# Kernel optimization log

Hardware: AMD Instinct MI355X
Metric: run time of the kernel (lower is better)

Reference implementation:

```python
import jax, jax.numpy as jnp
import numpy as np
import math

HQ, HKV, DH, WIN = 16, 4, 128, 512
RMS_EPS = 1.1920929e-07  # torch F.rms_norm default eps = fp32 machine eps


def _apply_rope(x, cos, sin):
    # x: [B,H,T,Dh]; interleaved-pair rotation as in the torch code
    x_even = x[..., ::2]
    x_odd = x[..., 1::2]
    x_rot = jnp.stack((-x_odd, x_even), axis=-1).reshape(x.shape)
    return x * cos + x_rot * sin


def _rms_norm(x):
    return x * jax.lax.rsqrt(jnp.mean(x * x, axis=-1, keepdims=True) + RMS_EPS)


def setup_inputs() -> dict:
    key = jax.random.key(0)
    k1, k2, k3 = jax.random.split(key, 3)
    B, T, C = 2, 2048, 2048
    x = jax.random.normal(k1, (B, T, C), dtype=jnp.float32)
    w_qkv = jax.random.normal(k2, ((HQ + 2 * HKV) * DH, C), dtype=jnp.float32) * 0.02
    w_proj = jax.random.normal(k3, (C, C), dtype=jnp.float32) * 0.02
    return {"x": x, "w_qkv": w_qkv, "w_proj": w_proj}


def reference(x, w_qkv, w_proj):
    B, T, C = x.shape
    rep = HQ // HKV
    qkv = x @ w_qkv.T  # [B,T,(Hq+2Hkv)*Dh]
    q, k, v = jnp.split(qkv, [HQ * DH, (HQ + HKV) * DH], axis=-1)
    Q = q.reshape(B, T, HQ, DH).transpose(0, 2, 1, 3)   # [B,Hq,T,Dh]
    K = k.reshape(B, T, HKV, DH).transpose(0, 2, 1, 3)  # [B,Hkv,T,Dh]
    V = v.reshape(B, T, HKV, DH).transpose(0, 2, 1, 3)
    # GQA expansion (repeat_interleave on head dim)
    K = jnp.repeat(K, rep, axis=1)
    V = jnp.repeat(V, rep, axis=1)
    # RoPE tables: freqs [T, Dh/2] -> cos/sin [1,1,T,Dh] via repeat_interleave(2)
    inv_freq = 1.0 / (10000.0 ** (jnp.arange(0, DH, 2, dtype=jnp.float32) / DH))
    freqs = jnp.arange(T, dtype=jnp.float32)[:, None] * inv_freq[None, :]
    cos = jnp.repeat(jnp.cos(freqs), 2, axis=-1)[None, None]
    sin = jnp.repeat(jnp.sin(freqs), 2, axis=-1)[None, None]
    Q = _rms_norm(_apply_rope(Q, cos, sin))
    K = _rms_norm(_apply_rope(K, cos, sin))
    scores = jnp.einsum('bhqd,bhkd->bhqk', Q, K) / math.sqrt(DH)
    i = jnp.arange(T)[:, None]
    j = jnp.arange(T)[None, :]
    mask = (i >= j) & ((i - j) < WIN)  # causal sliding window
    scores = jnp.where(mask[None, None], scores, -jnp.inf)
    attn = jax.nn.softmax(scores, axis=-1)
    y = jnp.einsum('bhqk,bhkd->bhqd', attn, V)
    y = y.transpose(0, 2, 1, 3).reshape(B, T, C)
    return y @ w_proj.T
```

## Files before the change

### kernel.cpp

```cpp
#include <hip/hip_runtime.h>
#include <stdint.h>

#define T_SEQ 2048
#define NB    2
#define DHD   128
#define NHQ   16
#define NHKV  4
#define SWIN  512
#define CDIM  2048
#define QKVN  3072
#define GBK   32

typedef __attribute__((ext_vector_type(8))) short short8;
typedef __attribute__((ext_vector_type(4))) float f32x4;
typedef __attribute__((ext_vector_type(16))) float f32x16;
typedef __attribute__((ext_vector_type(4))) unsigned int u32x4;
typedef __attribute__((address_space(3))) unsigned int lds_u32;
typedef __attribute__((address_space(1))) const unsigned int gbl_u32;

__device__ __forceinline__ unsigned short f2bf(float f) {
  unsigned int u = __float_as_uint(f);
  u += 0x7fffu + ((u >> 16) & 1u);
  return (unsigned short)(u >> 16);
}
__device__ __forceinline__ float bf2f(unsigned int h) {
  return __uint_as_float(h << 16);
}
__device__ __forceinline__ float exp2_fast(float x) {
  float r;
  asm("v_exp_f32 %0, %1" : "=v"(r) : "v"(x));
  return r;
}

__global__ __launch_bounds__(256) void k_f2bf3(const float* __restrict__ a, unsigned short* __restrict__ oa, int na4,
                                               const float* __restrict__ b, unsigned short* __restrict__ ob, int nb4,
                                               const float* __restrict__ c, unsigned short* __restrict__ oc, int nc4) {
  const int n = na4 + nb4 + nc4;
  for (int i = blockIdx.x * 256 + threadIdx.x; i < n; i += gridDim.x * 256) {
    const float* src; unsigned short* dst; int j = i;
    if (j < na4) { src = a; dst = oa; }
    else if (j < na4 + nb4) { j -= na4; src = b; dst = ob; }
    else { j -= na4 + nb4; src = c; dst = oc; }
    float4 v = reinterpret_cast<const float4*>(src)[j];
    uint2 o;
    o.x = ((unsigned int)f2bf(v.y) << 16) | f2bf(v.x);
    o.y = ((unsigned int)f2bf(v.w) << 16) | f2bf(v.z);
    reinterpret_cast<uint2*>(dst)[j] = o;
  }
}

__global__ __launch_bounds__(256) void k_trig(float* __restrict__ tbl) {
  int i = blockIdx.x * 256 + threadIdx.x;
  if (i >= T_SEQ * 64) return;
  int t = i >> 6, f = i & 63;
  float invf = powf(10000.f, -(float)f * (1.f / 64.f));
  float ang = (float)t * invf;
  tbl[i] = cosf(ang);
  tbl[T_SEQ * 64 + i] = sinf(ang);
}

template<int OUT_BF16>
__global__ __launch_bounds__(512, 2) void k_gemm192(const unsigned short* __restrict__ A,
                                                    const unsigned short* __restrict__ B,
                                                    void* __restrict__ Cout,
                                                    int M, int N, int K, int nbx) {
  extern __shared__ __align__(16) char lds[];
  const int tid = threadIdx.x, lane = tid & 63, wid = tid >> 6;
  const int lr = lane & 15, lg = lane >> 4;
  const int wr = wid >> 2, wcn = wid & 3;

  const int nwg = gridDim.x, cpx = nwg >> 3;
  const int id = (int)blockIdx.x;
  const int sid = (id & 7) * cpx + (id >> 3);
  const int by = sid / nbx, bx = sid - by * nbx;

  const unsigned short* Ab = A + (size_t)by * 256 * K;
  const unsigned short* Bb = B + (size_t)bx * 192 * K;

  const int row0 = tid >> 2;
  const int blk  = tid & 3;
  const int col0 = ((blk * 16) ^ (((row0 >> 1) & 3) << 4)) >> 1;
  const unsigned short* pA0 = Ab + (size_t)row0 * K + col0;
  const unsigned short* pA1 = pA0 + (size_t)128 * K;
  const unsigned short* pB0 = Bb + (size_t)row0 * K + col0;
  const unsigned short* pB2 = pB0 + (size_t)128 * K;

  const int sw  = ((lg ^ ((lr >> 1) & 3)) << 4);
  const int arb = (wr * 128 + lr) * 64 + sw;
  const int brb = 16384 + (wcn * 48 + lr) * 64 + sw;

  f32x4 acc[8][3];
#pragma unroll
  for (int mi = 0; mi < 8; ++mi)
#pragma unroll
    for (int ni = 0; ni < 3; ++ni)
#pragma unroll
      for (int r = 0; r < 4; ++r) acc[mi][ni][r] = 0.f;

#define STAGE(t) do {                                                                  \
    const int sl_ = (t) & 3; const int ko_ = (t) * GBK;                                \
    char* sb_ = lds + sl_ * 28672;                                                     \
    __builtin_amdgcn_global_load_lds((gbl_u32*)(pA0 + ko_),                            \
        (lds_u32*)(sb_ + wid * 1024), 16, 0, 0);                                       \
    __builtin_amdgcn_global_load_lds((gbl_u32*)(pA1 + ko_),                            \
        (lds_u32*)(sb_ + 8192 + wid * 1024), 16, 0, 0);                                \
    __builtin_amdgcn_global_load_lds((gbl_u32*)(pB0 + ko_),                            \
        (lds_u32*)(sb_ + 16384 + wid * 1024), 16, 0, 0);                               \
    if (wid < 4)                                                                       \
      __builtin_amdgcn_global_load_lds((gbl_u32*)(pB2 + ko_),                          \
          (lds_u32*)(sb_ + 24576 + wid * 1024), 16, 0, 0);                             \
  } while (0)

#define COMPUTE(t) do {                                                                \
    const int sl_ = (t) & 3;                                                           \
    const char* sb_ = lds + sl_ * 28672;                                               \
    short8 afr[8], bfr[3];                                                             \
    _Pragma("unroll") for (int mi = 0; mi < 8; ++mi)                                   \
      afr[mi] = *reinterpret_cast<const short8*>(sb_ + arb + mi * 1024);               \
    _Pragma("unroll") for (int ni = 0; ni < 3; ++ni)                                   \
      bfr[ni] = *reinterpret_cast<const short8*>(sb_ + brb + ni * 1024);               \
    __builtin_amdgcn_s_setprio(1);                                                     \
    _Pragma("unroll") for (int mi = 0; mi < 8; ++mi)                                   \
      _Pragma("unroll") for (int ni = 0; ni < 3; ++ni)                                 \
        acc[mi][ni] = __builtin_amdgcn_mfma_f32_16x16x32_bf16(afr[mi], bfr[ni],        \
                                                              acc[mi][ni], 0, 0, 0);   \
    __builtin_amdgcn_s_setprio(0);                                                     \
  } while (0)

#define WAITBAR2(nlo, nhi) do {                                                        \
    if (wid < 4) asm volatile("s_waitcnt vmcnt(" #nlo ")" ::: "memory");               \
    else         asm volatile("s_waitcnt vmcnt(" #nhi ")" ::: "memory");               \
    __builtin_amdgcn_s_barrier();                                                      \
    asm volatile("" ::: "memory");                                                     \
  } while (0)

  const int nt = K / GBK;
  STAGE(0); STAGE(1); STAGE(2);
  for (int t = 0; t < nt - 3; ++t) {
    WAITBAR2(10, 8);
    STAGE(t + 3);
    COMPUTE(t);
  }
  WAITBAR2(10, 8); COMPUTE(nt - 3);
  WAITBAR2(5, 4);  COMPUTE(nt - 2);
  WAITBAR2(0, 0);  COMPUTE(nt - 1);

#undef STAGE
#undef COMPUTE
#undef WAITBAR2

#pragma unroll
  for (int mi = 0; mi < 8; ++mi) {
    const int row0c = by * 256 + wr * 128 + mi * 16 + lg * 4;
#pragma unroll
    for (int ni = 0; ni < 3; ++ni) {
      const int col = bx * 192 + wcn * 48 + ni * 16 + lr;
#pragma unroll
      for (int r = 0; r < 4; ++r) {
        size_t idx = (size_t)(row0c + r) * N + col;
        if (OUT_BF16) ((unsigned short*)Cout)[idx] = f2bf(acc[mi][ni][r]);
        else          ((float*)Cout)[idx] = acc[mi][ni][r];
      }
    }
  }
}

template<int OUT_BF16>
__global__ __launch_bounds__(512) void k_gemm128(const unsigned short* __restrict__ A,
                                                 const unsigned short* __restrict__ B,
                                                 void* __restrict__ Cout,
                                                 int M, int N, int K, int nbx) {
  extern __shared__ __align__(16) char lds[];
  const int tid = threadIdx.x, lane = tid & 63, wid = tid >> 6;
  const int lr = lane & 15, lg = lane >> 4;
  const int wr = wid >> 2, wcn = wid & 3;

  const int nwg = gridDim.x, cpx = nwg >> 3;
  const int id = (int)blockIdx.x;
  const int sid = (id & 7) * cpx + (id >> 3);
  const int by = sid / nbx, bx = sid - by * nbx;

  const unsigned short* Ab = A + (size_t)by * 128 * K;
  const unsigned short* Bb = B + (size_t)bx * 256 * K;

  const int row0 = tid >> 2;
  const int blk  = tid & 3;
  const int col0 = ((blk * 16) ^ (((row0 >> 1) & 3) << 4)) >> 1;
  const unsigned short* pA0 = Ab + (size_t)row0 * K + col0;
  const unsigned short* pB0 = Bb + (size_t)row0 * K + col0;
  const unsigned short* pB1 = pB0 + (size_t)128 * K;

  const int sw  = ((lg ^ ((lr >> 1) & 3)) << 4);
  const int arb = (wr * 64 + lr) * 64 + sw;
  const int brb = (wcn * 64 + lr) * 64 + sw;

  f32x4 acc[4][4];
#pragma unroll
  for (int mi = 0; mi < 4; ++mi)
#pragma unroll
    for (int ni = 0; ni < 4; ++ni)
#pragma unroll
      for (int r = 0; r < 4; ++r) acc[mi][ni][r] = 0.f;

#define STAGE(t, sl_) do {                                                             \
    const int ko_ = (t) * GBK;                                                         \
    __builtin_amdgcn_global_load_lds((gbl_u32*)(pA0 + ko_),                            \
        (lds_u32*)(lds + (sl_) * 24576 + wid * 1024), 16, 0, 0);                       \
    __builtin_amdgcn_global_load_lds((gbl_u32*)(pB0 + ko_),                            \
        (lds_u32*)(lds + (sl_) * 24576 + 8192 + wid * 1024), 16, 0, 0);                \
    __builtin_amdgcn_global_load_lds((gbl_u32*)(pB1 + ko_),                            \
        (lds_u32*)(lds + (sl_) * 24576 + 16384 + wid * 1024), 16, 0, 0);               \
  } while (0)

#define COMPUTE(sl_) do {                                                              \
    const char* As_ = lds + (sl_) * 24576;                                             \
    const char* Bs_ = As_ + 8192;                                                      \
    short8 afr[4], bfr[4];                                                             \
    _Pragma("unroll") for (int mi = 0; mi < 4; ++mi)                                   \
      afr[mi] = *reinterpret_cast<const short8*>(As_ + arb + mi * 1024);               \
    _Pragma("unroll") for (int ni = 0; ni < 4; ++ni)                                   \
      bfr[ni] = *reinterpret_cast<const short8*>(Bs_ + brb + ni * 1024);               \
    __builtin_amdgcn_s_setprio(1);                                                     \
    _Pragma("unroll") for (int mi = 0; mi < 4; ++mi)                                   \
      _Pragma("unroll") for (int ni = 0; ni < 4; ++ni)                                 \
        acc[mi][ni] = __builtin_amdgcn_mfma_f32_16x16x32_bf16(afr[mi], bfr[ni],        \
                                                              acc[mi][ni], 0, 0, 0);   \
    __builtin_amdgcn_s_setprio(0);                                                     \
  } while (0)

#define WAITBAR(n) do {                                                                \
    asm volatile("s_waitcnt vmcnt(" #n ")" ::: "memory");                              \
    __builtin_amdgcn_s_barrier();                                                      \
    asm volatile("" ::: "memory");                                                     \
  } while (0)

  const int nt = K / GBK;
  STAGE(0, 0); STAGE(1, 1);
  int sc = 0, ss = 2;
  for (int t = 0; t < nt - 2; ++t) {
    WAITBAR(3);
    STAGE(t + 2, ss);
    COMPUTE(sc);
    sc = (sc == 2) ? 0 : sc + 1;
    ss = (ss == 2) ? 0 : ss + 1;
  }
  WAITBAR(3);
  COMPUTE(sc);
  sc = (sc == 2) ? 0 : sc + 1;
  WAITBAR(0);
  COMPUTE(sc);

#undef STAGE
#undef COMPUTE
#undef WAITBAR

#pragma unroll
  for (int mi = 0; mi < 4; ++mi) {
    const int row0c = by * 128 + wr * 64 + mi * 16 + lg * 4;
#pragma unroll
    for (int ni = 0; ni < 4; ++ni) {
      const int col = bx * 256 + wcn * 64 + ni * 16 + lr;
#pragma unroll
      for (int r = 0; r < 4; ++r) {
        size_t idx = (size_t)(row0c + r) * N + col;
        if (OUT_BF16) ((unsigned short*)Cout)[idx] = f2bf(acc[mi][ni][r]);
        else          ((float*)Cout)[idx] = acc[mi][ni][r];
      }
    }
  }
}

__global__ __launch_bounds__(256) void k_rope_rms(const unsigned short* __restrict__ qkv,
                                                  const float* __restrict__ tbl,
                                                  unsigned short* __restrict__ Qo,
                                                  unsigned short* __restrict__ Ko) {
  const int lane = threadIdx.x & 63, wid = threadIdx.x >> 6;
  const int job = blockIdx.x * 4 + wid;
  const int row = job / 20;
  const int hh  = job - row * 20;
  const int b = row >> 11, t = row & (T_SEQ - 1);
  const unsigned short* src;
  unsigned short* dst;
  float scale;
  if (hh < NHQ) {
    src = qkv + (size_t)row * QKVN + hh * DHD;
    dst = Qo + (((size_t)b * NHQ + hh) * T_SEQ + t) * DHD;
    scale = 0.1275173019f;
  } else {
    int h = hh - NHQ;
    src = qkv + (size_t)row * QKVN + CDIM + h * DHD;
    dst = Ko + (((size_t)b * NHKV + h) * T_SEQ + t) * DHD;
    scale = 1.f;
  }
  unsigned int pr = *reinterpret_cast<const unsigned int*>(src + lane * 2);
  float xe = bf2f(pr & 0xffffu), xo = bf2f(pr >> 16);
  float c = tbl[t * 64 + lane], s = tbl[T_SEQ * 64 + t * 64 + lane];
  float e = xe * c - xo * s;
  float o = xo * c + xe * s;
  float ss = e * e + o * o;
#pragma unroll
  for (int off = 1; off < 64; off <<= 1) ss += __shfl_xor(ss, off);
  float rn = rsqrtf(ss * (1.f / 128.f) + 1.1920929e-07f) * scale;
  unsigned short eb = f2bf(e * rn), ob = f2bf(o * rn);
  *reinterpret_cast<unsigned int*>(dst + lane * 2) = ((unsigned int)ob << 16) | eb;
}

__global__ __launch_bounds__(256) void k_vtrans(const unsigned short* __restrict__ qkv,
                                                unsigned short* __restrict__ Vt) {
  __shared__ unsigned short tile[64][65];
  const int blk = blockIdx.x;
  const int dt = blk & 1;
  const int tt = (blk >> 1) & 31;
  const int h = (blk >> 6) & 3;
  const int b = blk >> 8;
  const int t0 = tt * 64, d0 = dt * 64;
#pragma unroll
  for (int i = 0; i < 16; ++i) {
    int idx = i * 256 + threadIdx.x;
    int tl = idx >> 6, dl = idx & 63;
    tile[tl][dl] = qkv[(size_t)(b * T_SEQ + t0 + tl) * QKVN + (CDIM + NHKV * DHD) + h * DHD + d0 + dl];
  }
  __syncthreads();
#pragma unroll
  for (int i = 0; i < 16; ++i) {
    int idx = i * 256 + threadIdx.x;
    int dl = idx >> 6, tl = idx & 63;
    Vt[((size_t)(b * NHKV + h) * DHD + d0 + dl) * T_SEQ + t0 + tl] = tile[tl][dl];
  }
}

__global__ __launch_bounds__(512) void k_attn(const unsigned short* __restrict__ Q,
                                              const unsigned short* __restrict__ K,
                                              const unsigned short* __restrict__ Vt,
                                              unsigned short* __restrict__ Y) {
  __shared__ __align__(16) char lds[65536];
  const int tid = threadIdx.x, lane = tid & 63, wid = tid >> 6;
  const int l31 = lane & 31, hi = lane >> 5;

  const int id = (int)blockIdx.x;
  const int sid = (id & 7) * 32 + (id >> 3);
  const int qt = sid & 7;
  const int h = (sid >> 3) & 15;
  const int b = sid >> 7;
  const int hkv = h >> 2;
  const int q0 = qt * 256;
  const int q0g = q0 + wid * 32;

  const unsigned short* Qp = Q + (((size_t)b * NHQ + h) * T_SEQ + q0g) * DHD;
  const char* Kbyte = (const char*)(K + ((size_t)b * NHKV + hkv) * T_SEQ * DHD);
  const char* Vbyte = (const char*)(Vt + ((size_t)b * NHKV + hkv) * DHD * T_SEQ);

  const int ksrc = (tid >> 4) * 256 + (((tid & 15) * 16) ^ (((tid >> 4) & 7) << 4));
  const int vsrc = (tid >> 2) * 4096 + (((tid & 3) * 16) ^ (((tid >> 2) & 3) << 4));

  const int ksw = (l31 & 7) << 4;
  const int vsw = (l31 & 3) << 4;

#define STAGEKV(k0_, sb_) do {                                                           \
    const char* kt_ = Kbyte + (size_t)(k0_) * 256;                                       \
    const char* vt_ = Vbyte + (size_t)(k0_) * 2;                                         \
    __builtin_amdgcn_global_load_lds((gbl_u32*)(kt_ + ksrc),                             \
        (lds_u32*)(lds + (sb_) + wid * 1024), 16, 0, 0);                                 \
    __builtin_amdgcn_global_load_lds((gbl_u32*)(vt_ + vsrc),                             \
        (lds_u32*)(lds + (sb_) + 8192 + wid * 1024), 16, 0, 0);                          \
  } while (0)

  const int kt0 = (q0 >= SWIN) ? ((q0 - (SWIN - 1)) >> 5) : 0;
  const int kth = (q0 + 255) >> 5;

  STAGEKV(kt0 * 32, 0);

  short8 qf[8];
#pragma unroll
  for (int ds = 0; ds < 8; ++ds)
    qf[ds] = *reinterpret_cast<const short8*>(Qp + (size_t)l31 * DHD + ds * 16 + hi * 8);

  f32x16 accO[4];
#pragma unroll
  for (int dt = 0; dt < 4; ++dt)
#pragma unroll
    for (int r = 0; r < 16; ++r) accO[dt][r] = 0.f;
  float m = -1e30f, l = 0.f;
  const int qg = q0g + l31;

  int sl = 0;
  for (int t = kt0; t <= kth; ++t) {
    const int sln = (sl == 2) ? 0 : sl + 1;
    if (t < kth) {
      STAGEKV((t + 1) * 32, sln * 16384);
      asm volatile("s_waitcnt vmcnt(2)" ::: "memory");
    } else {
      asm volatile("s_waitcnt vmcnt(0)" ::: "memory");
    }
    __builtin_amdgcn_s_barrier();

    const int k0 = t * 32;
    if (k0 <= q0g && k0 + 31 >= q0g - (SWIN - 1)) {
      const char* kbase = lds + sl * 16384;
      const char* vbase = kbase + 8192;

      short8 kf[8];
#pragma unroll
      for (int ds = 0; ds < 8; ++ds)
        kf[ds] = *reinterpret_cast<const short8*>(kbase + l31 * 256 + ((ds * 32 + hi * 16) ^ ksw));

      f32x16 s;
#pragma unroll
      for (int r = 0; r < 16; ++r) s[r] = 0.f;
      __builtin_amdgcn_s_setprio(1);
#pragma unroll
      for (int ds = 0; ds < 8; ++ds)
        s = __builtin_amdgcn_mfma_f32_32x32x16_bf16(kf[ds], qf[ds], s, 0, 0, 0);
      __builtin_amdgcn_s_setprio(0);

      if (k0 < q0g - 480 || k0 >= q0g) {
#pragma unroll
        for (int r = 0; r < 16; ++r) {
          int kk = k0 + (r & 3) + 8 * (r >> 2) + 4 * hi;
          if (kk > qg || qg - kk >= SWIN) s[r] = -1e30f;
        }
      }

      float mx[8];
#pragma unroll
      for (int j = 0; j < 8; ++j) mx[j] = fmaxf(s[2 * j], s[2 * j + 1]);
      float a0 = fmaxf(mx[0], mx[1]), a1 = fmaxf(mx[2], mx[3]);
      float a2 = fmaxf(mx[4], mx[5]), a3 = fmaxf(mx[6], mx[7]);
      float tmax = fmaxf(fmaxf(a0, a1), fmaxf(a2, a3));
      tmax = fmaxf(tmax, __shfl_xor(tmax, 32));

      float mn = m;
      if (!__all(tmax <= m + 8.f)) {
        mn = fmaxf(m, tmax);
        float alpha = exp2_fast(m - mn);
        l *= alpha;
#pragma unroll
        for (int dt = 0; dt < 4; ++dt)
#pragma unroll
          for (int r = 0; r < 16; ++r) accO[dt][r] *= alpha;
        m = mn;
      }

#pragma unroll
      for (int r = 0; r < 16; ++r) s[r] = exp2_fast(s[r] - mn);
      float sx[8];
#pragma unroll
      for (int j = 0; j < 8; ++j) sx[j] = s[2 * j] + s[2 * j + 1];
      float b0 = sx[0] + sx[1], b1 = sx[2] + sx[3], b2 = sx[4] + sx[5], b3 = sx[6] + sx[7];
      float ps = (b0 + b1) + (b2 + b3);
      ps += __shfl_xor(ps, 32);
      l += ps;

      unsigned int w[8];
#pragma unroll
      for (int j = 0; j < 8; ++j)
        asm("v_cvt_pk_bf16_f32 %0, %1, %2" : "=v"(w[j]) : "v"(s[2 * j]), "v"(s[2 * j + 1]));
      asm("v_permlane32_swap_b32 %0, %1" : "+v"(w[0]), "+v"(w[2]));
      asm("v_permlane32_swap_b32 %0, %1" : "+v"(w[1]), "+v"(w[3]));
      asm("v_permlane32_swap_b32 %0, %1" : "+v"(w[4]), "+v"(w[6]));
      asm("v_permlane32_swap_b32 %0, %1" : "+v"(w[5]), "+v"(w[7]));
      u32x4 p0 = {w[0], w[1], w[2], w[3]};
      u32x4 p1 = {w[4], w[5], w[6], w[7]};
      short8 pf0 = __builtin_bit_cast(short8, p0);
      short8 pf1 = __builtin_bit_cast(short8, p1);

      __builtin_amdgcn_s_setprio(1);
#pragma unroll
      for (int dt = 0; dt < 4; ++dt) {
        const char* vrow = vbase + (dt * 2048 + l31 * 64);
        short8 vf0 = *reinterpret_cast<const short8*>(vrow + ((hi * 16) ^ vsw));
        short8 vf1 = *reinterpret_cast<const short8*>(vrow + ((32 + hi * 16) ^ vsw));
        accO[dt] = __builtin_amdgcn_mfma_f32_32x32x16_bf16(vf0, pf0, accO[dt], 0, 0, 0);
        accO[dt] = __builtin_amdgcn_mfma_f32_32x32x16_bf16(vf1, pf1, accO[dt], 0, 0, 0);
      }
      __builtin_amdgcn_s_setprio(0);
    }
    sl = sln;
  }
#undef STAGEKV

  __syncthreads();

  float inv = 1.f / l;
  char* obc = lds + wid * 8192;
#pragma unroll
  for (int dt = 0; dt < 4; ++dt)
#pragma unroll
    for (int j = 0; j < 8; ++j) {
      float a = accO[dt][2 * j] * inv, c = accO[dt][2 * j + 1] * inv;
      unsigned int wv;
      asm("v_cvt_pk_bf16_f32 %0, %1, %2" : "=v"(wv) : "v"(a), "v"(c));
      int d = dt * 32 + 2 * (j & 1) + 8 * (j >> 1) + 4 * hi;
      *reinterpret_cast<unsigned int*>(obc + l31 * 256 + ((d * 2) ^ ksw)) = wv;
    }
#pragma unroll
  for (int i = 0; i < 8; ++i) {
    int chunk = i * 64 + lane;
    int row = chunk >> 4, c8 = chunk & 15;
    short8 v = *reinterpret_cast<const short8*>(obc + row * 256 + ((c8 * 16) ^ ((row & 7) << 4)));
    *reinterpret_cast<short8*>(Y + ((size_t)b * T_SEQ + q0g + row) * CDIM + h * DHD + c8 * 8) = v;
  }
}

extern "C" void kernel_launch(void* const* d_in, const int* in_sizes, int n_in,
                              void* d_out, int out_size, void* d_ws, size_t ws_size,
                              hipStream_t stream) {
  const float* x     = (const float*)d_in[0];
  const float* wqkv  = (const float*)d_in[1];
  const float* wproj = (const float*)d_in[2];
  float* out = (float*)d_out;

  char* ws = (char*)d_ws;
  unsigned short* xb     = (unsigned short*)(ws + 0);
  unsigned short* wqkvb  = (unsigned short*)(ws + 16777216);
  unsigned short* wprojb = (unsigned short*)(ws + 29360128);
  unsigned short* qkvb   = (unsigned short*)(ws + 37748736);
  unsigned short* Qb     = (unsigned short*)(ws + 62914560);
  unsigned short* Kb     = (unsigned short*)(ws + 79691776);
  unsigned short* Vtb    = (unsigned short*)(ws + 83886080);
  float* tbl             = (float*)(ws + 88080384);
  unsigned short* yb     = xb;

  k_f2bf3<<<2048, 256, 0, stream>>>(x, xb, (NB * T_SEQ * CDIM) / 4,
                                    wqkv, wqkvb, (QKVN * CDIM) / 4,
                                    wproj, wprojb, (CDIM * CDIM) / 4);
  k_trig<<<(T_SEQ * 64 + 255) / 256, 256, 0, stream>>>(tbl);

  k_gemm192<1><<<256, 512, 114688, stream>>>(
      xb, wqkvb, qkvb, NB * T_SEQ, QKVN, CDIM, QKVN / 192);
  k_rope_rms<<<(NB * T_SEQ * (NHQ + NHKV)) / 4, 256, 0, stream>>>(qkvb, tbl, Qb, Kb);
  k_vtrans<<<NB * NHKV * 32 * 2, 256, 0, stream>>>(qkvb, Vtb);
  k_attn<<<NB * NHQ * (T_SEQ / 256), 512, 0, stream>>>(Qb, Kb, Vtb, yb);
  k_gemm128<0><<<256, 512, 73728, stream>>>(
      yb, wprojb, out, NB * T_SEQ, CDIM, CDIM, CDIM / 256);
}
```

Baseline: 167.2 us.

## Fuse trig into convert, merge rope with V transpose, deepen proj GEMM K-tile

The RoPE table computation now runs inside the fp32-to-bf16 conversion kernel, and the rope/RMS and V-transpose kernels are merged into one launch with block-range dispatch. Together these cut two kernel launches and their tail gaps. The output-projection GEMM doubles its K tile from 32 to 64 with a new 128-byte-row XOR swizzle. That halves the number of barrier iterations, at the cost of LDS use rising to 144KB, which limits blocks per CU.

Result: faster. 161.1 us (-3.7%).

```diff
diff --git a/kernel.cpp b/kernel.cpp
--- a/kernel.cpp
+++ b/kernel.cpp
@@ -32,9 +32,18 @@
   return r;
 }
 
-__global__ __launch_bounds__(256) void k_f2bf3(const float* __restrict__ a, unsigned short* __restrict__ oa, int na4,
-                                               const float* __restrict__ b, unsigned short* __restrict__ ob, int nb4,
-                                               const float* __restrict__ c, unsigned short* __restrict__ oc, int nc4) {
+__global__ __launch_bounds__(256) void k_f2bf3t(const float* __restrict__ a, unsigned short* __restrict__ oa, int na4,
+                                                const float* __restrict__ b, unsigned short* __restrict__ ob, int nb4,
+                                                const float* __restrict__ c, unsigned short* __restrict__ oc, int nc4,
+                                                float* __restrict__ tbl) {
+  if (blockIdx.x < 512) {
+    int i = blockIdx.x * 256 + threadIdx.x;
+    int t = i >> 6, f = i & 63;
+    float invf = powf(10000.f, -(float)f * (1.f / 64.f));
+    float ang = (float)t * invf;
+    tbl[i] = cosf(ang);
+    tbl[T_SEQ * 64 + i] = sinf(ang);
+  }
   const int n = na4 + nb4 + nc4;
   for (int i = blockIdx.x * 256 + threadIdx.x; i < n; i += gridDim.x * 256) {
     const float* src; unsigned short* dst; int j = i;
@@ -47,16 +56,6 @@
     o.y = ((unsigned int)f2bf(v.w) << 16) | f2bf(v.z);
     reinterpret_cast<uint2*>(dst)[j] = o;
   }
-}
-
-__global__ __launch_bounds__(256) void k_trig(float* __restrict__ tbl) {
-  int i = blockIdx.x * 256 + threadIdx.x;
-  if (i >= T_SEQ * 64) return;
-  int t = i >> 6, f = i & 63;
-  float invf = powf(10000.f, -(float)f * (1.f / 64.f));
-  float ang = (float)t * invf;
-  tbl[i] = cosf(ang);
-  tbl[T_SEQ * 64 + i] = sinf(ang);
 }
 
 template<int OUT_BF16>
@@ -166,10 +165,10 @@
 }
 
 template<int OUT_BF16>
-__global__ __launch_bounds__(512) void k_gemm128(const unsigned short* __restrict__ A,
-                                                 const unsigned short* __restrict__ B,
-                                                 void* __restrict__ Cout,
-                                                 int M, int N, int K, int nbx) {
+__global__ __launch_bounds__(512) void k_gemm128b(const unsigned short* __restrict__ A,
+                                                  const unsigned short* __restrict__ B,
+                                                  void* __restrict__ Cout,
+                                                  int M, int N, int K, int nbx) {
   extern __shared__ __align__(16) char lds[];
   const int tid = threadIdx.x, lane = tid & 63, wid = tid >> 6;
   const int lr = lane & 15, lg = lane >> 4;
@@ -183,16 +182,16 @@
   const unsigned short* Ab = A + (size_t)by * 128 * K;
   const unsigned short* Bb = B + (size_t)bx * 256 * K;
 
-  const int row0 = tid >> 2;
-  const int blk  = tid & 3;
-  const int col0 = ((blk * 16) ^ (((row0 >> 1) & 3) << 4)) >> 1;
-  const unsigned short* pA0 = Ab + (size_t)row0 * K + col0;
-  const unsigned short* pB0 = Bb + (size_t)row0 * K + col0;
-  const unsigned short* pB1 = pB0 + (size_t)128 * K;
-
-  const int sw  = ((lg ^ ((lr >> 1) & 3)) << 4);
-  const int arb = (wr * 64 + lr) * 64 + sw;
-  const int brb = (wcn * 64 + lr) * 64 + sw;
+  const int trow = tid >> 3;
+  const int tc   = tid & 7;
+  const int csw  = (((tc * 16) ^ ((trow & 7) << 4)) >> 1);
+  const unsigned short* pA = Ab + (size_t)trow * K + csw;
+  const unsigned short* pB = Bb + (size_t)trow * K + csw;
+
+  const int arb = (wr * 64 + lr) * 128;
+  const int brb = 16384 + (wcn * 64 + lr) * 128;
+  const int ch0 = (lg * 16) ^ ((lr & 7) << 4);
+  const int ch1 = (64 + lg * 16) ^ ((lr & 7) << 4);
 
   f32x4 acc[4][4];
 #pragma unroll
@@ -202,29 +201,37 @@
 #pragma unroll
       for (int r = 0; r < 4; ++r) acc[mi][ni][r] = 0.f;
 
-#define STAGE(t, sl_) do {                                                             \
-    const int ko_ = (t) * GBK;                                                         \
-    __builtin_amdgcn_global_load_lds((gbl_u32*)(pA0 + ko_),                            \
-        (lds_u32*)(lds + (sl_) * 24576 + wid * 1024), 16, 0, 0);                       \
-    __builtin_amdgcn_global_load_lds((gbl_u32*)(pB0 + ko_),                            \
-        (lds_u32*)(lds + (sl_) * 24576 + 8192 + wid * 1024), 16, 0, 0);                \
-    __builtin_amdgcn_global_load_lds((gbl_u32*)(pB1 + ko_),                            \
-        (lds_u32*)(lds + (sl_) * 24576 + 16384 + wid * 1024), 16, 0, 0);               \
+#define STAGE(t_, sl_) do {                                                            \
+    const unsigned short* at_ = pA + (size_t)(t_) * 64;                                \
+    const unsigned short* bt_ = pB + (size_t)(t_) * 64;                                \
+    char* sb_ = lds + (sl_) * 49152;                                                   \
+    _Pragma("unroll") for (int i = 0; i < 2; ++i)                                      \
+      __builtin_amdgcn_global_load_lds((gbl_u32*)(at_ + (size_t)i * 64 * K),           \
+          (lds_u32*)(sb_ + i * 8192 + wid * 1024), 16, 0, 0);                          \
+    _Pragma("unroll") for (int j = 0; j < 4; ++j)                                      \
+      __builtin_amdgcn_global_load_lds((gbl_u32*)(bt_ + (size_t)j * 64 * K),           \
+          (lds_u32*)(sb_ + 16384 + j * 8192 + wid * 1024), 16, 0, 0);                  \
   } while (0)
 
 #define COMPUTE(sl_) do {                                                              \
-    const char* As_ = lds + (sl_) * 24576;                                             \
-    const char* Bs_ = As_ + 8192;                                                      \
-    short8 afr[4], bfr[4];                                                             \
-    _Pragma("unroll") for (int mi = 0; mi < 4; ++mi)                                   \
-      afr[mi] = *reinterpret_cast<const short8*>(As_ + arb + mi * 1024);               \
-    _Pragma("unroll") for (int ni = 0; ni < 4; ++ni)                                   \
-      bfr[ni] = *reinterpret_cast<const short8*>(Bs_ + brb + ni * 1024);               \
+    const char* sb_ = lds + (sl_) * 49152;                                             \
+    short8 afr[4][2], bfr[4][2];                                                       \
+    _Pragma("unroll") for (int mi = 0; mi < 4; ++mi) {                                 \
+      afr[mi][0] = *reinterpret_cast<const short8*>(sb_ + arb + mi * 2048 + ch0);      \
+      afr[mi][1] = *reinterpret_cast<const short8*>(sb_ + arb + mi * 2048 + ch1);      \
+    }                                                                                  \
+    _Pragma("unroll") for (int ni = 0; ni < 4; ++ni) {                                 \
+      bfr[ni][0] = *reinterpret_cast<const short8*>(sb_ + brb + ni * 2048 + ch0);      \
+      bfr[ni][1] = *reinterpret_cast<const short8*>(sb_ + brb + ni * 2048 + ch1);      \
+    }                                                                                  \
     __builtin_amdgcn_s_setprio(1);                                                     \
     _Pragma("unroll") for (int mi = 0; mi < 4; ++mi)                                   \
-      _Pragma("unroll") for (int ni = 0; ni < 4; ++ni)                                 \
-        acc[mi][ni] = __builtin_amdgcn_mfma_f32_16x16x32_bf16(afr[mi], bfr[ni],        \
-                                                              acc[mi][ni], 0, 0, 0);   \
+      _Pragma("unroll") for (int ni = 0; ni < 4; ++ni) {                               \
+        f32x4 a_ = acc[mi][ni];                                                        \
+        a_ = __builtin_amdgcn_mfma_f32_16x16x32_bf16(afr[mi][0], bfr[ni][0], a_, 0, 0, 0); \
+        a_ = __builtin_amdgcn_mfma_f32_16x16x32_bf16(afr[mi][1], bfr[ni][1], a_, 0, 0, 0); \
+        acc[mi][ni] = a_;                                                              \
+      }                                                                                \
     __builtin_amdgcn_s_setprio(0);                                                     \
   } while (0)
 
@@ -234,17 +241,17 @@
     asm volatile("" ::: "memory");                                                     \
   } while (0)
 
-  const int nt = K / GBK;
+  const int nt = K >> 6;
   STAGE(0, 0); STAGE(1, 1);
   int sc = 0, ss = 2;
   for (int t = 0; t < nt - 2; ++t) {
-    WAITBAR(3);
+    WAITBAR(6);
     STAGE(t + 2, ss);
     COMPUTE(sc);
     sc = (sc == 2) ? 0 : sc + 1;
     ss = (ss == 2) ? 0 : ss + 1;
   }
-  WAITBAR(3);
+  WAITBAR(6);
   COMPUTE(sc);
   sc = (sc == 2) ? 0 : sc + 1;
   WAITBAR(0);
@@ -270,62 +277,63 @@
   }
 }
 
-__global__ __launch_bounds__(256) void k_rope_rms(const unsigned short* __restrict__ qkv,
-                                                  const float* __restrict__ tbl,
-                                                  unsigned short* __restrict__ Qo,
-                                                  unsigned short* __restrict__ Ko) {
-  const int lane = threadIdx.x & 63, wid = threadIdx.x >> 6;
-  const int job = blockIdx.x * 4 + wid;
-  const int row = job / 20;
-  const int hh  = job - row * 20;
-  const int b = row >> 11, t = row & (T_SEQ - 1);
-  const unsigned short* src;
-  unsigned short* dst;
-  float scale;
-  if (hh < NHQ) {
-    src = qkv + (size_t)row * QKVN + hh * DHD;
-    dst = Qo + (((size_t)b * NHQ + hh) * T_SEQ + t) * DHD;
-    scale = 0.1275173019f;
+#define NRB ((NB * T_SEQ * (NHQ + NHKV)) / 4)
+__global__ __launch_bounds__(256) void k_rope_vt(const unsigned short* __restrict__ qkv,
+                                                 const float* __restrict__ tbl,
+                                                 unsigned short* __restrict__ Qo,
+                                                 unsigned short* __restrict__ Ko,
+                                                 unsigned short* __restrict__ Vt) {
+  __shared__ unsigned short tile[64][65];
+  if ((int)blockIdx.x < NRB) {
+    const int lane = threadIdx.x & 63, wid = threadIdx.x >> 6;
+    const int job = blockIdx.x * 4 + wid;
+    const int row = job / 20;
+    const int hh  = job - row * 20;
+    const int b = row >> 11, t = row & (T_SEQ - 1);
+    const unsigned short* src;
+    unsigned short* dst;
+    float scale;
+    if (hh < NHQ) {
+      src = qkv + (size_t)row * QKVN + hh * DHD;
+      dst = Qo + (((size_t)b * NHQ + hh) * T_SEQ + t) * DHD;
+      scale = 0.1275173019f;
+    } else {
+      int h = hh - NHQ;
+      src = qkv + (size_t)row * QKVN + CDIM + h * DHD;
+      dst = Ko + (((size_t)b * NHKV + h) * T_SEQ + t) * DHD;
+      scale = 1.f;
+    }
+    unsigned int pr = *reinterpret_cast<const unsigned int*>(src + lane * 2);
+    float xe = bf2f(pr & 0xffffu), xo = bf2f(pr >> 16);
+    float c = tbl[t * 64 + lane], s = tbl[T_SEQ * 64 + t * 64 + lane];
+    float e = xe * c - xo * s;
+    float o = xo * c + xe * s;
+    float ss = e * e + o * o;
+#pragma unroll
+    for (int off = 1; off < 64; off <<= 1) ss += __shfl_xor(ss, off);
+    float rn = rsqrtf(ss * (1.f / 128.f) + 1.1920929e-07f) * scale;
+    unsigned short eb = f2bf(e * rn), ob = f2bf(o * rn);
+    *reinterpret_cast<unsigned int*>(dst + lane * 2) = ((unsigned int)ob << 16) | eb;
   } else {
-    int h = hh - NHQ;
-    src = qkv + (size_t)row * QKVN + CDIM + h * DHD;
-    dst = Ko + (((size_t)b * NHKV + h) * T_SEQ + t) * DHD;
-    scale = 1.f;
-  }
-  unsigned int pr = *reinterpret_cast<const unsigned int*>(src + lane * 2);
-  float xe = bf2f(pr & 0xffffu), xo = bf2f(pr >> 16);
-  float c = tbl[t * 64 + lane], s = tbl[T_SEQ * 64 + t * 64 + lane];
-  float e = xe * c - xo * s;
-  float o = xo * c + xe * s;
-  float ss = e * e + o * o;
-#pragma unroll
-  for (int off = 1; off < 64; off <<= 1) ss += __shfl_xor(ss, off);
-  float rn = rsqrtf(ss * (1.f / 128.f) + 1.1920929e-07f) * scale;
-  unsigned short eb = f2bf(e * rn), ob = f2bf(o * rn);
-  *reinterpret_cast<unsigned int*>(dst + lane * 2) = ((unsigned int)ob << 16) | eb;
-}
-
-__global__ __launch_bounds__(256) void k_vtrans(const unsigned short* __restrict__ qkv,
-                                                unsigned short* __restrict__ Vt) {
-  __shared__ unsigned short tile[64][65];
-  const int blk = blockIdx.x;
-  const int dt = blk & 1;
-  const int tt = (blk >> 1) & 31;
-  const int h = (blk >> 6) & 3;
-  const int b = blk >> 8;
-  const int t0 = tt * 64, d0 = dt * 64;
-#pragma unroll
-  for (int i = 0; i < 16; ++i) {
-    int idx = i * 256 + threadIdx.x;
-    int tl = idx >> 6, dl = idx & 63;
-    tile[tl][dl] = qkv[(size_t)(b * T_SEQ + t0 + tl) * QKVN + (CDIM + NHKV * DHD) + h * DHD + d0 + dl];
-  }
-  __syncthreads();
-#pragma unroll
-  for (int i = 0; i < 16; ++i) {
-    int idx = i * 256 + threadIdx.x;
-    int dl = idx >> 6, tl = idx & 63;
-    Vt[((size_t)(b * NHKV + h) * DHD + d0 + dl) * T_SEQ + t0 + tl] = tile[tl][dl];
+    const int blk = (int)blockIdx.x - NRB;
+    const int dt = blk & 1;
+    const int tt = (blk >> 1) & 31;
+    const int h = (blk >> 6) & 3;
+    const int b = blk >> 8;
+    const int t0 = tt * 64, d0 = dt * 64;
+#pragma unroll
+    for (int i = 0; i < 16; ++i) {
+      int idx = i * 256 + threadIdx.x;
+      int tl = idx >> 6, dl = idx & 63;
+      tile[tl][dl] = qkv[(size_t)(b * T_SEQ + t0 + tl) * QKVN + (CDIM + NHKV * DHD) + h * DHD + d0 + dl];
+    }
+    __syncthreads();
+#pragma unroll
+    for (int i = 0; i < 16; ++i) {
+      int idx = i * 256 + threadIdx.x;
+      int dl = idx >> 6, tl = idx & 63;
+      Vt[((size_t)(b * NHKV + h) * DHD + d0 + dl) * T_SEQ + t0 + tl] = tile[tl][dl];
+    }
   }
 }
 
@@ -521,16 +529,14 @@
   float* tbl             = (float*)(ws + 88080384);
   unsigned short* yb     = xb;
 
-  k_f2bf3<<<2048, 256, 0, stream>>>(x, xb, (NB * T_SEQ * CDIM) / 4,
-                                    wqkv, wqkvb, (QKVN * CDIM) / 4,
-                                    wproj, wprojb, (CDIM * CDIM) / 4);
-  k_trig<<<(T_SEQ * 64 + 255) / 256, 256, 0, stream>>>(tbl);
+  k_f2bf3t<<<2048, 256, 0, stream>>>(x, xb, (NB * T_SEQ * CDIM) / 4,
+                                     wqkv, wqkvb, (QKVN * CDIM) / 4,
+                                     wproj, wprojb, (CDIM * CDIM) / 4, tbl);
 
   k_gemm192<1><<<256, 512, 114688, stream>>>(
       xb, wqkvb, qkvb, NB * T_SEQ, QKVN, CDIM, QKVN / 192);
-  k_rope_rms<<<(NB * T_SEQ * (NHQ + NHKV)) / 4, 256, 0, stream>>>(qkvb, tbl, Qb, Kb);
-  k_vtrans<<<NB * NHKV * 32 * 2, 256, 0, stream>>>(qkvb, Vtb);
+  k_rope_vt<<<NRB + 512, 256, 0, stream>>>(qkvb, tbl, Qb, Kb, Vtb);
   k_attn<<<NB * NHQ * (T_SEQ / 256), 512, 0, stream>>>(Qb, Kb, Vtb, yb);
-  k_gemm128<0><<<256, 512, 73728, stream>>>(
+  k_gemm128b<0><<<256, 512, 147456, stream>>>(
       yb, wprojb, out, NB * T_SEQ, CDIM, CDIM, CDIM / 256);
 }
```
